# Performance work log

Measured on AMD Instinct MI355X. Metric: run time of the kernel, lower is better.

The kernel has to match this reference:

```python
import jax, jax.numpy as jnp
import numpy as np

B, T_EN, T_DE, D_EN, D_DE, UNITS = 16, 256, 256, 512, 512, 128


def setup_inputs() -> dict:
    key = jax.random.key(0)
    k1, k2, k3, k4, k5 = jax.random.split(key, 5)
    # glorot-uniform style scale for weights
    def glorot(k, shape):
        lim = np.sqrt(6.0 / (shape[0] + shape[1]))
        return jax.random.uniform(k, shape, jnp.float32, -lim, lim)
    return {
        "en_seq": jax.random.normal(k1, (B, T_EN, D_EN), jnp.float32),
        "de_seq": jax.random.normal(k2, (B, T_DE, D_DE), jnp.float32),
        "w_en": glorot(k3, (D_EN, UNITS)),
        "w_de": glorot(k4, (D_DE, UNITS)),
        "nu": glorot(k5, (UNITS, 1)),
    }


def reference(en_seq, de_seq, w_en, w_de, nu):
    # Additive (Bahdanau) time attention.
    # Original keras code builds the (de, en) cross product via K.repeat /
    # K.repeat_elements with de-major, en-minor ordering; equivalent to
    # broadcasting att_de over a new en axis and att_en over a new de axis.
    att_en = jnp.einsum("bie,eu->biu", en_seq, w_en)   # (B, T_en, U)
    att_de = jnp.einsum("bjd,du->bju", de_seq, w_de)   # (B, T_de, U)
    # co_m: (B, T_de, T_en, U) — the large broadcast intermediate
    co_m = jnp.tanh(att_de[:, :, None, :] + att_en[:, None, :, :])
    mu = jnp.einsum("bjiu,u->bji", co_m, nu[:, 0])      # (B, T_de, T_en)
    alphas = jax.nn.softmax(mu, axis=-1)                # softmax over encoder time
    sum_en = jnp.einsum("bji,bie->bje", alphas, en_seq)  # (B, T_de, D_en)
    return jnp.concatenate([de_seq, sum_en], axis=-1)    # (B, T_de, D_de + D_en)
```

## Files before the change

kernel.cpp:

```cpp
#include <hip/hip_runtime.h>
#include <hip/hip_bf16.h>

#define TANH_SCALE 2.8853900817779268f

__global__ __launch_bounds__(256, 2) void proj2_kernel(
        const float* __restrict__ en, const float* __restrict__ de,
        const float* __restrict__ w_en, const float* __restrict__ w_de,
        float* __restrict__ att_en, float* __restrict__ att_de) {
    const float* X;
    const float* W;
    float* OUT;
    if (blockIdx.y == 0) { X = en; W = w_en; OUT = att_en; }
    else                 { X = de; W = w_de; OUT = att_de; }

    __shared__ float w_sh[64][128];
    __shared__ float x_sh[16][64];
    const int tid  = threadIdx.x;
    const int u    = tid & 127;
    const int half = tid >> 7;
    const int row0 = blockIdx.x * 16;

    float acc[8];
#pragma unroll
    for (int r = 0; r < 8; ++r) acc[r] = 0.0f;

    for (int kt = 0; kt < 512; kt += 64) {
        const float4* Wg = reinterpret_cast<const float4*>(W + (size_t)kt * 128);
        float4* wsh4 = reinterpret_cast<float4*>(&w_sh[0][0]);
#pragma unroll
        for (int t = 0; t < 8; ++t) wsh4[tid + 256 * t] = Wg[tid + 256 * t];
        {
            int r = tid >> 4, kk4 = (tid & 15) * 4;
            reinterpret_cast<float4*>(&x_sh[0][0])[tid] =
                *reinterpret_cast<const float4*>(X + (size_t)(row0 + r) * 512 + kt + kk4);
        }
        __syncthreads();
#pragma unroll
        for (int kk = 0; kk < 64; kk += 4) {
            float w0 = w_sh[kk][u], w1 = w_sh[kk + 1][u];
            float w2 = w_sh[kk + 2][u], w3 = w_sh[kk + 3][u];
#pragma unroll
            for (int r = 0; r < 8; ++r) {
                float4 x4 = *reinterpret_cast<const float4*>(&x_sh[half * 8 + r][kk]);
                acc[r] = fmaf(x4.x, w0, acc[r]);
                acc[r] = fmaf(x4.y, w1, acc[r]);
                acc[r] = fmaf(x4.z, w2, acc[r]);
                acc[r] = fmaf(x4.w, w3, acc[r]);
            }
        }
        __syncthreads();
    }
#pragma unroll
    for (int r = 0; r < 8; ++r)
        OUT[(size_t)(row0 + half * 8 + r) * 128 + u] = acc[r] * TANH_SCALE;
}

__global__ __launch_bounds__(256, 2) void fused_attn_kernel(
        const float* __restrict__ att_en, const float* __restrict__ att_de,
        const float* __restrict__ nu, const float* __restrict__ en,
        const float* __restrict__ de, float* __restrict__ out) {
    const int phys = blockIdx.x;
    const int lid  = (phys & 7) * 64 + (phys >> 3);
    const int b    = lid >> 5;
    const int j0   = (lid & 31) * 8;
    const int tid  = threadIdx.x;

    __shared__ float de_sh[8][128];
    __shared__ float nu_sh[128];
    __shared__ float al[8][256];
    __shared__ float red[4][8];

    reinterpret_cast<float4*>(&de_sh[0][0])[tid] =
        reinterpret_cast<const float4*>(att_de + ((size_t)b * 256 + j0) * 128)[tid];
    if (tid < 128) nu_sh[tid] = nu[tid];

    {
        const float4* dsrc =
            reinterpret_cast<const float4*>(de + ((size_t)b * 256 + j0) * 512);
#pragma unroll
        for (int t = 0; t < 4; ++t) {
            int idx = tid + 256 * t;
            int j = idx >> 7, c4 = idx & 127;
            reinterpret_cast<float4*>(out + (size_t)(b * 256 + j0 + j) * 1024)[c4] =
                dsrc[idx];
        }
    }
    __syncthreads();

    float s[8];
#pragma unroll
    for (int j = 0; j < 8; ++j) s[j] = 0.0f;
    const float4* en4 =
        reinterpret_cast<const float4*>(att_en + ((size_t)b * 256 + tid) * 128);
    for (int q = 0; q < 4; ++q) {
        float ev[32];
#pragma unroll
        for (int t = 0; t < 8; ++t) {
            float4 v = en4[q * 8 + t];
            ev[4 * t] = v.x; ev[4 * t + 1] = v.y;
            ev[4 * t + 2] = v.z; ev[4 * t + 3] = v.w;
        }
#pragma unroll
        for (int uu = 0; uu < 32; ++uu) {
            float nuv = nu_sh[q * 32 + uu];
#pragma unroll
            for (int j = 0; j < 8; ++j) {
                float x = ev[uu] + de_sh[j][q * 32 + uu];
                float e = __builtin_exp2f(-x);
                float r = __builtin_amdgcn_rcpf(1.0f + e);
                float t = fmaf(-e, r, r);
                s[j] = fmaf(t, nuv, s[j]);
            }
        }
    }

    float p[8];
#pragma unroll
    for (int j = 0; j < 8; ++j) p[j] = __expf(s[j]);
    float tot[8];
#pragma unroll
    for (int j = 0; j < 8; ++j) {
        float t = p[j];
#pragma unroll
        for (int off = 32; off >= 1; off >>= 1) t += __shfl_xor(t, off);
        tot[j] = t;
    }
    const int lane = tid & 63, wv = tid >> 6;
    if (lane == 0) {
#pragma unroll
        for (int j = 0; j < 8; ++j) red[wv][j] = tot[j];
    }
    __syncthreads();
#pragma unroll
    for (int j = 0; j < 8; ++j) {
        float T = red[0][j] + red[1][j] + red[2][j] + red[3][j];
        al[j][tid] = p[j] * __builtin_amdgcn_rcpf(T);
    }
    __syncthreads();

    float acc0[8], acc1[8];
#pragma unroll
    for (int j = 0; j < 8; ++j) { acc0[j] = 0.0f; acc1[j] = 0.0f; }
    const float* enb = en + (size_t)b * 256 * 512;
    for (int i0 = 0; i0 < 256; i0 += 4) {
        float a[8][4];
#pragma unroll
        for (int j = 0; j < 8; ++j) {
            float4 v = *reinterpret_cast<const float4*>(&al[j][i0]);
            a[j][0] = v.x; a[j][1] = v.y; a[j][2] = v.z; a[j][3] = v.w;
        }
#pragma unroll
        for (int ii = 0; ii < 4; ++ii) {
            float e0 = enb[(size_t)(i0 + ii) * 512 + tid];
            float e1 = enb[(size_t)(i0 + ii) * 512 + tid + 256];
#pragma unroll
            for (int j = 0; j < 8; ++j) {
                acc0[j] = fmaf(a[j][ii], e0, acc0[j]);
                acc1[j] = fmaf(a[j][ii], e1, acc1[j]);
            }
        }
    }
#pragma unroll
    for (int j = 0; j < 8; ++j) {
        size_t row = (size_t)(b * 256 + j0 + j);
        out[row * 1024 + 512 + tid] = acc0[j];
        out[row * 1024 + 768 + tid] = acc1[j];
    }
}

extern "C" void kernel_launch(void* const* d_in, const int* in_sizes, int n_in,
                              void* d_out, int out_size, void* d_ws, size_t ws_size,
                              hipStream_t stream) {
    const float* en   = (const float*)d_in[0];
    const float* de   = (const float*)d_in[1];
    const float* w_en = (const float*)d_in[2];
    const float* w_de = (const float*)d_in[3];
    const float* nu   = (const float*)d_in[4];
    float* out = (float*)d_out;

    char* ws = (char*)d_ws;
    float* att_en = (float*)(ws);
    float* att_de = (float*)(ws + (size_t)4096 * 128 * 4);

    proj2_kernel<<<dim3(256, 2), 256, 0, stream>>>(en, de, w_en, w_de,
                                                   att_en, att_de);
    fused_attn_kernel<<<dim3(512), 256, 0, stream>>>(att_en, att_de, nu,
                                                     en, de, out);
}
```

Before: 193.8 us.

## Factor tanh via precomputed exponentials and double threads in attention kernel

```diff
diff --git a/kernel.cpp b/kernel.cpp
--- a/kernel.cpp
+++ b/kernel.cpp
@@ -3,33 +3,31 @@
 
 #define TANH_SCALE 2.8853900817779268f
 
-__global__ __launch_bounds__(256, 2) void proj2_kernel(
+__global__ __launch_bounds__(256, 4) void proj2_kernel(
         const float* __restrict__ en, const float* __restrict__ de,
         const float* __restrict__ w_en, const float* __restrict__ w_de,
-        float* __restrict__ att_en, float* __restrict__ att_de) {
+        float* __restrict__ Een, float* __restrict__ Ede) {
     const float* X;
     const float* W;
     float* OUT;
-    if (blockIdx.y == 0) { X = en; W = w_en; OUT = att_en; }
-    else                 { X = de; W = w_de; OUT = att_de; }
+    if (blockIdx.y == 0) { X = en; W = w_en; OUT = Een; }
+    else                 { X = de; W = w_de; OUT = Ede; }
 
     __shared__ float w_sh[64][128];
-    __shared__ float x_sh[16][64];
+    __shared__ float x_sh[8][64];
     const int tid  = threadIdx.x;
     const int u    = tid & 127;
     const int half = tid >> 7;
-    const int row0 = blockIdx.x * 16;
+    const int row0 = blockIdx.x * 8;
 
-    float acc[8];
-#pragma unroll
-    for (int r = 0; r < 8; ++r) acc[r] = 0.0f;
+    float acc[4] = {0.0f, 0.0f, 0.0f, 0.0f};
 
     for (int kt = 0; kt < 512; kt += 64) {
         const float4* Wg = reinterpret_cast<const float4*>(W + (size_t)kt * 128);
         float4* wsh4 = reinterpret_cast<float4*>(&w_sh[0][0]);
 #pragma unroll
         for (int t = 0; t < 8; ++t) wsh4[tid + 256 * t] = Wg[tid + 256 * t];
-        {
+        if (tid < 128) {
             int r = tid >> 4, kk4 = (tid & 15) * 4;
             reinterpret_cast<float4*>(&x_sh[0][0])[tid] =
                 *reinterpret_cast<const float4*>(X + (size_t)(row0 + r) * 512 + kt + kk4);
@@ -40,8 +38,8 @@
             float w0 = w_sh[kk][u], w1 = w_sh[kk + 1][u];
             float w2 = w_sh[kk + 2][u], w3 = w_sh[kk + 3][u];
 #pragma unroll
-            for (int r = 0; r < 8; ++r) {
-                float4 x4 = *reinterpret_cast<const float4*>(&x_sh[half * 8 + r][kk]);
+            for (int r = 0; r < 4; ++r) {
+                float4 x4 = *reinterpret_cast<const float4*>(&x_sh[half * 4 + r][kk]);
                 acc[r] = fmaf(x4.x, w0, acc[r]);
                 acc[r] = fmaf(x4.y, w1, acc[r]);
                 acc[r] = fmaf(x4.z, w2, acc[r]);
@@ -51,12 +49,13 @@
         __syncthreads();
     }
 #pragma unroll
-    for (int r = 0; r < 8; ++r)
-        OUT[(size_t)(row0 + half * 8 + r) * 128 + u] = acc[r] * TANH_SCALE;
+    for (int r = 0; r < 4; ++r)
+        OUT[(size_t)(row0 + half * 4 + r) * 128 + u] =
+            __builtin_exp2f(-TANH_SCALE * acc[r]);
 }
 
-__global__ __launch_bounds__(256, 2) void fused_attn_kernel(
-        const float* __restrict__ att_en, const float* __restrict__ att_de,
+__global__ __launch_bounds__(512, 4) void fused_attn_kernel(
+        const float* __restrict__ Een, const float* __restrict__ Ede,
         const float* __restrict__ nu, const float* __restrict__ en,
         const float* __restrict__ de, float* __restrict__ out) {
     const int phys = blockIdx.x;
@@ -64,22 +63,25 @@
     const int b    = lid >> 5;
     const int j0   = (lid & 31) * 8;
     const int tid  = threadIdx.x;
+    const int i    = tid & 255;
+    const int uh   = tid >> 8;
 
-    __shared__ float de_sh[8][128];
-    __shared__ float nu_sh[128];
+    __shared__ float ede_sh[8][128];
+    __shared__ float nu2_sh[128];
     __shared__ float al[8][256];
-    __shared__ float red[4][8];
+    __shared__ float red[8][4];
 
-    reinterpret_cast<float4*>(&de_sh[0][0])[tid] =
-        reinterpret_cast<const float4*>(att_de + ((size_t)b * 256 + j0) * 128)[tid];
-    if (tid < 128) nu_sh[tid] = nu[tid];
+    if (tid < 256)
+        reinterpret_cast<float4*>(&ede_sh[0][0])[tid] =
+            reinterpret_cast<const float4*>(Ede + ((size_t)b * 256 + j0) * 128)[tid];
+    if (tid >= 256 && tid < 384) nu2_sh[tid - 256] = 2.0f * nu[tid - 256];
 
     {
         const float4* dsrc =
             reinterpret_cast<const float4*>(de + ((size_t)b * 256 + j0) * 512);
 #pragma unroll
-        for (int t = 0; t < 4; ++t) {
-            int idx = tid + 256 * t;
+        for (int t = 0; t < 2; ++t) {
+            int idx = tid + 512 * t;
             int j = idx >> 7, c4 = idx & 127;
             reinterpret_cast<float4*>(out + (size_t)(b * 256 + j0 + j) * 1024)[c4] =
                 dsrc[idx];
@@ -87,61 +89,62 @@
     }
     __syncthreads();
 
-    float s[8];
+    float s[4] = {0.0f, 0.0f, 0.0f, 0.0f};
+    const float4* e4 =
+        reinterpret_cast<const float4*>(Een + ((size_t)b * 256 + i) * 128);
+    for (int q = 0; q < 8; ++q) {
+        float ev[16], nv[16];
 #pragma unroll
-    for (int j = 0; j < 8; ++j) s[j] = 0.0f;
-    const float4* en4 =
-        reinterpret_cast<const float4*>(att_en + ((size_t)b * 256 + tid) * 128);
-    for (int q = 0; q < 4; ++q) {
-        float ev[32];
-#pragma unroll
-        for (int t = 0; t < 8; ++t) {
-            float4 v = en4[q * 8 + t];
-            ev[4 * t] = v.x; ev[4 * t + 1] = v.y;
-            ev[4 * t + 2] = v.z; ev[4 * t + 3] = v.w;
+        for (int t = 0; t < 4; ++t) {
+            float4 a = e4[q * 4 + t];
+            ev[4 * t] = a.x; ev[4 * t + 1] = a.y; ev[4 * t + 2] = a.z; ev[4 * t + 3] = a.w;
+            float4 n = *reinterpret_cast<const float4*>(&nu2_sh[q * 16 + 4 * t]);
+            nv[4 * t] = n.x; nv[4 * t + 1] = n.y; nv[4 * t + 2] = n.z; nv[4 * t + 3] = n.w;
         }
 #pragma unroll
-        for (int uu = 0; uu < 32; ++uu) {
-            float nuv = nu_sh[q * 32 + uu];
+        for (int jl = 0; jl < 4; ++jl) {
+            const int j = uh * 4 + jl;
+            float dv[16];
 #pragma unroll
-            for (int j = 0; j < 8; ++j) {
-                float x = ev[uu] + de_sh[j][q * 32 + uu];
-                float e = __builtin_exp2f(-x);
+            for (int t = 0; t < 4; ++t) {
+                float4 d = *reinterpret_cast<const float4*>(&ede_sh[j][q * 16 + 4 * t]);
+                dv[4 * t] = d.x; dv[4 * t + 1] = d.y; dv[4 * t + 2] = d.z; dv[4 * t + 3] = d.w;
+            }
+#pragma unroll
+            for (int t = 0; t < 16; ++t) {
+                float e = ev[t] * dv[t];
                 float r = __builtin_amdgcn_rcpf(1.0f + e);
-                float t = fmaf(-e, r, r);
-                s[j] = fmaf(t, nuv, s[j]);
+                s[jl] = fmaf(nv[t], r, s[jl]);
             }
         }
     }
 
-    float p[8];
+    float p[4];
 #pragma unroll
-    for (int j = 0; j < 8; ++j) p[j] = __expf(s[j]);
-    float tot[8];
+    for (int jl = 0; jl < 4; ++jl) p[jl] = __expf(s[jl]);
+    const int lane = tid & 63;
+    const int w    = (tid >> 6) & 3;
 #pragma unroll
-    for (int j = 0; j < 8; ++j) {
-        float t = p[j];
+    for (int jl = 0; jl < 4; ++jl) {
+        float t = p[jl];
 #pragma unroll
         for (int off = 32; off >= 1; off >>= 1) t += __shfl_xor(t, off);
-        tot[j] = t;
-    }
-    const int lane = tid & 63, wv = tid >> 6;
-    if (lane == 0) {
-#pragma unroll
-        for (int j = 0; j < 8; ++j) red[wv][j] = tot[j];
+        if (lane == 0) red[uh * 4 + jl][w] = t;
     }
     __syncthreads();
 #pragma unroll
-    for (int j = 0; j < 8; ++j) {
-        float T = red[0][j] + red[1][j] + red[2][j] + red[3][j];
-        al[j][tid] = p[j] * __builtin_amdgcn_rcpf(T);
+    for (int jl = 0; jl < 4; ++jl) {
+        const int j = uh * 4 + jl;
+        float T = red[j][0] + red[j][1] + red[j][2] + red[j][3];
+        al[j][i] = p[jl] * __builtin_amdgcn_rcpf(T);
     }
     __syncthreads();
 
-    float acc0[8], acc1[8];
+    float acc[8];
 #pragma unroll
-    for (int j = 0; j < 8; ++j) { acc0[j] = 0.0f; acc1[j] = 0.0f; }
+    for (int j = 0; j < 8; ++j) acc[j] = 0.0f;
     const float* enb = en + (size_t)b * 256 * 512;
+    const int c = tid;
     for (int i0 = 0; i0 < 256; i0 += 4) {
         float a[8][4];
 #pragma unroll
@@ -151,20 +154,16 @@
         }
 #pragma unroll
         for (int ii = 0; ii < 4; ++ii) {
-            float e0 = enb[(size_t)(i0 + ii) * 512 + tid];
-            float e1 = enb[(size_t)(i0 + ii) * 512 + tid + 256];
+            float e0 = enb[(size_t)(i0 + ii) * 512 + c];
 #pragma unroll
-            for (int j = 0; j < 8; ++j) {
-                acc0[j] = fmaf(a[j][ii], e0, acc0[j]);
-                acc1[j] = fmaf(a[j][ii], e1, acc1[j]);
-            }
+            for (int j = 0; j < 8; ++j)
+                acc[j] = fmaf(a[j][ii], e0, acc[j]);
         }
     }
 #pragma unroll
     for (int j = 0; j < 8; ++j) {
         size_t row = (size_t)(b * 256 + j0 + j);
-        out[row * 1024 + 512 + tid] = acc0[j];
-        out[row * 1024 + 768 + tid] = acc1[j];
+        out[row * 1024 + 512 + c] = acc[j];
     }
 }
 
@@ -179,11 +178,9 @@
     float* out = (float*)d_out;
 
     char* ws = (char*)d_ws;
-    float* att_en = (float*)(ws);
-    float* att_de = (float*)(ws + (size_t)4096 * 128 * 4);
+    float* Een = (float*)(ws);
+    float* Ede = (float*)(ws + (size_t)4096 * 128 * 4);
 
-    proj2_kernel<<<dim3(256, 2), 256, 0, stream>>>(en, de, w_en, w_de,
-                                                   att_en, att_de);
-    fused_attn_kernel<<<dim3(512), 256, 0, stream>>>(att_en, att_de, nu,
-                                                     en, de, out);
+    proj2_kernel<<<dim3(512, 2), 256, 0, stream>>>(en, de, w_en, w_de, Een, Ede);
+    fused_attn_kernel<<<dim3(512), 512, 0, stream>>>(Een, Ede, nu, en, de, out);
 }
```

After: 163.8 us. 1.18x faster.
